# Kernel optimization log

Hardware: AMD Instinct MI355X
Metric: run time of the kernel (lower is better)

The kernel has to match this reference:

```python
import jax, jax.numpy as jnp
import numpy as np


def setup_inputs() -> dict:
    key = jax.random.key(0)
    ks = jax.random.split(key, 4)
    B, S, D, E = 8, 4096, 2048, 64
    scale = 1.0 / np.sqrt(D)
    return {
        "x": jax.random.normal(ks[0], (B, S, D), dtype=jnp.float32),
        "W_route": jax.random.normal(ks[1], (E, D), dtype=jnp.float32) * scale,
        "b_route": jnp.zeros((E,), dtype=jnp.float32),
        "W_noise": jax.random.normal(ks[2], (E, D), dtype=jnp.float32) * scale,
        "b_noise": jnp.zeros((E,), dtype=jnp.float32),
        "noise_eps": jax.random.normal(ks[3], (B, S, E), dtype=jnp.float32),
    }


TOP_K = 2


def reference(x, W_route, b_route, W_noise, b_noise, noise_eps):
    # Dual linear projections: [B,S,D] @ [D,E] -> [B,S,E]
    logits = jnp.einsum("bsd,ed->bse", x, W_route) + b_route
    noise_logits = jnp.einsum("bsd,ed->bse", x, W_noise) + b_noise
    noisy_logits = logits + noise_eps * jax.nn.softplus(noise_logits)

    B, S, E = noisy_logits.shape
    flat = noisy_logits.reshape(B * S, E)
    top_vals, top_idx = jax.lax.top_k(flat, TOP_K)  # [N,K]

    # Scatter top-k values into -inf background, then softmax over experts.
    neg_inf = jnp.full_like(flat, -jnp.inf)
    rows = jnp.arange(B * S)[:, None]
    sparse = neg_inf.at[rows, top_idx].set(top_vals)
    router_output = jax.nn.softmax(sparse, axis=-1).reshape(B, S, E)
    indices = top_idx.reshape(B, S, TOP_K)
    return router_output, indices
```

## Files before the change

kernel.cpp:

```cpp
#include <hip/hip_runtime.h>
#include <math.h>

typedef _Float16 f16;
typedef __attribute__((ext_vector_type(8))) _Float16 half8;
typedef __attribute__((ext_vector_type(4))) float f32x4;

#define NEXP 64
#define TM 64
#define L_STRIDE 132

__device__ __forceinline__ float softplus_f(float x) {
    return fmaxf(x, 0.0f) + log1pf(expf(-fabsf(x)));
}

__device__ __forceinline__ void lds_dma16(const void* g, void* l) {
    __builtin_amdgcn_global_load_lds(
        (const __attribute__((address_space(1))) unsigned int*)g,
        (__attribute__((address_space(3))) unsigned int*)l, 16, 0, 0);
}

__device__ __forceinline__ void cvt_split(const float4 a, const float4 b,
                                          half8& hv, half8& lv) {
    const float vv[8] = {a.x, a.y, a.z, a.w, b.x, b.y, b.z, b.w};
#pragma unroll
    for (int j = 0; j < 8; ++j) {
        const f16 h = (f16)vv[j];
        hv[j] = h;
        lv[j] = (f16)((vv[j] - (float)h) * 4096.0f);
    }
}

__global__ void wsplit_kernel(const float* __restrict__ Wr,
                              const float* __restrict__ Wn,
                              f16* __restrict__ ws, int D) {
    const int per_col = D >> 3;
    const int t = blockIdx.x * blockDim.x + threadIdx.x;
    const int col = t / per_col;
    const int k0  = (t - col * per_col) * 8;
    if (col >= 128) return;
    const float* src = (col < NEXP) ? &Wr[(size_t)col * D] : &Wn[(size_t)(col - NEXP) * D];
    const float4 v0 = *(const float4*)&src[k0];
    const float4 v1 = *(const float4*)&src[k0 + 4];
    half8 hi, lo;
    cvt_split(v0, v1, hi, lo);
    const int kc = k0 >> 5, q = (k0 >> 3) & 3;
    const size_t base = (size_t)kc * 8192 + (size_t)q * 1024 + (size_t)col * 8;
    *(half8*)&ws[base]        = hi;
    *(half8*)&ws[base + 4096] = lo;
}

__global__ __launch_bounds__(256, 3)
void router_mfma_kernel(const float* __restrict__ x,
                        const f16* __restrict__ wsW,
                        const float* __restrict__ br,
                        const float* __restrict__ bn,
                        const float* __restrict__ eps,
                        float* __restrict__ out,
                        int N, int D) {
    __shared__ union alignas(16) {
        struct { f16 B[2][8192]; f16 A[2][4096]; } st;
        float L[TM][L_STRIDE];
    } sm;
    __shared__ float biasLDS[128];
    __shared__ float p1s[TM], p2s[TM];
    __shared__ int   i1s[TM], i2s[TM];

    const int tid  = threadIdx.x;
    const int lane = tid & 63;
    const int w    = tid >> 6;
    const int rowbase = blockIdx.x * TM;
    const int wr = w & 1, wc = w >> 1;
    const int quad = lane >> 4;
    const int l16  = lane & 15;

    if (tid < 128) biasLDS[tid] = (tid < NEXP) ? br[tid] : bn[tid - NEXP];

    f32x4 accM[2][4], accC[2][4];
#pragma unroll
    for (int i = 0; i < 2; ++i)
#pragma unroll
        for (int j = 0; j < 4; ++j) {
            accM[i][j] = (f32x4){0.f, 0.f, 0.f, 0.f};
            accC[i][j] = (f32x4){0.f, 0.f, 0.f, 0.f};
        }

    const int sr = tid >> 2;
    const int sq = tid & 3;
    const float* xrow = &x[(size_t)(rowbase + sr) * D + sq * 8];
    const int nkc = D >> 5;

    float4 xva0, xva1, xvb0, xvb1;

    {
        const char* gsrc = (const char*)wsW + w * 4096 + lane * 16;
        char* ldst = (char*)&sm.st.B[0][0] + w * 4096;
#pragma unroll
        for (int i = 0; i < 4; ++i) lds_dma16(gsrc + i * 1024, ldst + i * 1024);
        __builtin_amdgcn_sched_barrier(0);
        const float4 c0a = *(const float4*)&xrow[0];
        const float4 c0b = *(const float4*)&xrow[4];
        __builtin_amdgcn_sched_barrier(0);
        xva0 = *(const float4*)&xrow[32];
        xva1 = *(const float4*)&xrow[36];
        xvb0 = *(const float4*)&xrow[64];
        xvb1 = *(const float4*)&xrow[68];
        __builtin_amdgcn_sched_barrier(0);
        half8 hv, lv;
        cvt_split(c0a, c0b, hv, lv);
        *(half8*)&sm.st.A[0][sq * 512 + sr * 8]        = hv;
        *(half8*)&sm.st.A[0][2048 + sq * 512 + sr * 8] = lv;
        asm volatile("s_waitcnt vmcnt(4) lgkmcnt(0)" : : : "memory");
        __builtin_amdgcn_s_barrier();
        __builtin_amdgcn_sched_barrier(0);
    }

#define KLOOP_BODY(KC, XV0, XV1)                                               \
    {                                                                          \
        const int cur = (KC) & 1, nxt = cur ^ 1;                               \
        if ((KC) + 1 < nkc) {                                                  \
            const char* gsrc = (const char*)wsW + (size_t)((KC) + 1) * 16384   \
                               + w * 4096 + lane * 16;                         \
            char* ldst = (char*)&sm.st.B[nxt][0] + w * 4096;                   \
            lds_dma16(gsrc,        ldst);                                      \
            lds_dma16(gsrc + 1024, ldst + 1024);                               \
            lds_dma16(gsrc + 2048, ldst + 2048);                               \
            lds_dma16(gsrc + 3072, ldst + 3072);                               \
        }                                                                      \
        __builtin_amdgcn_sched_barrier(0);                                     \
        if ((KC) + 1 < nkc) {                                                  \
            half8 hv, lv;                                                      \
            cvt_split(XV0, XV1, hv, lv);                                       \
            *(half8*)&sm.st.A[nxt][sq * 512 + sr * 8]        = hv;             \
            *(half8*)&sm.st.A[nxt][2048 + sq * 512 + sr * 8] = lv;             \
        }                                                                      \
        if ((KC) + 3 < nkc) {                                                  \
            XV0 = *(const float4*)&xrow[((KC) + 3) * 32];                      \
            XV1 = *(const float4*)&xrow[((KC) + 3) * 32 + 4];                  \
        }                                                                      \
        __builtin_amdgcn_sched_barrier(0);                                     \
        half8 ah[2], al[2], bh[4], bl[4];                                      \
        _Pragma("unroll")                                                      \
        for (int rt = 0; rt < 2; ++rt) {                                       \
            const int r = (wr * 32 + rt * 16 + l16) * 8;                       \
            ah[rt] = *(const half8*)&sm.st.A[cur][quad * 512 + r];             \
            al[rt] = *(const half8*)&sm.st.A[cur][2048 + quad * 512 + r];      \
        }                                                                      \
        _Pragma("unroll")                                                      \
        for (int ct = 0; ct < 4; ++ct) {                                       \
            const int c = (wc * 64 + ct * 16 + l16) * 8;                       \
            bh[ct] = *(const half8*)&sm.st.B[cur][quad * 1024 + c];            \
            bl[ct] = *(const half8*)&sm.st.B[cur][4096 + quad * 1024 + c];     \
        }                                                                      \
        _Pragma("unroll")                                                      \
        for (int rt = 0; rt < 2; ++rt)                                         \
            _Pragma("unroll")                                                  \
            for (int ct = 0; ct < 4; ++ct) {                                   \
                accM[rt][ct] = __builtin_amdgcn_mfma_f32_16x16x32_f16(         \
                    ah[rt], bh[ct], accM[rt][ct], 0, 0, 0);                    \
                accC[rt][ct] = __builtin_amdgcn_mfma_f32_16x16x32_f16(         \
                    al[rt], bh[ct], accC[rt][ct], 0, 0, 0);                    \
                accC[rt][ct] = __builtin_amdgcn_mfma_f32_16x16x32_f16(         \
                    ah[rt], bl[ct], accC[rt][ct], 0, 0, 0);                    \
            }                                                                  \
        if ((KC) + 3 < nkc)                                                    \
            asm volatile("s_waitcnt vmcnt(2) lgkmcnt(0)" : : : "memory");      \
        else                                                                   \
            asm volatile("s_waitcnt vmcnt(0) lgkmcnt(0)" : : : "memory");      \
        __builtin_amdgcn_s_barrier();                                          \
        __builtin_amdgcn_sched_barrier(0);                                     \
    }

    for (int kc = 0; kc < nkc; kc += 2) {
        KLOOP_BODY(kc,     xva0, xva1)
        KLOOP_BODY(kc + 1, xvb0, xvb1)
    }
#undef KLOOP_BODY

#pragma unroll
    for (int rt = 0; rt < 2; ++rt)
#pragma unroll
        for (int ct = 0; ct < 4; ++ct) {
            const int row = wr * 32 + rt * 16 + quad * 4;
            const int col = wc * 64 + ct * 16 + l16;
            const float bcol = biasLDS[col];
#pragma unroll
            for (int rg = 0; rg < 4; ++rg)
                sm.L[row + rg][col] = accM[rt][ct][rg] + accC[rt][ct][rg] * (1.0f / 4096.0f) + bcol;
        }
    __syncthreads();

#pragma unroll
    for (int t = 0; t < 4; ++t) {
        const int f   = tid * 4 + t * 1024;
        const int row = f >> 6;
        const int e0  = f & 63;
        const float4 ev = *(const float4*)&eps[(size_t)(rowbase + row) * NEXP + e0];
        const float evs[4] = {ev.x, ev.y, ev.z, ev.w};
#pragma unroll
        for (int j = 0; j < 4; ++j) {
            const float lg = sm.L[row][e0 + j];
            const float nz = sm.L[row][NEXP + e0 + j];
            sm.L[row][e0 + j] = fmaf(evs[j], softplus_f(nz), lg);
        }
    }
    __syncthreads();

    if (tid < TM) {
        const int r = tid;
        float v1t = -INFINITY, v2t = -INFINITY;
        int i1 = 0, i2 = 0;
#pragma unroll 8
        for (int e = 0; e < NEXP; ++e) {
            const float v = sm.L[r][e];
            if (v > v1t) { v2t = v1t; i2 = i1; v1t = v; i1 = e; }
            else if (v > v2t) { v2t = v; i2 = e; }
        }
        const float z = expf(v2t - v1t);
        const float s = 1.0f + z;
        p1s[r] = 1.0f / s;
        p2s[r] = z / s;
        i1s[r] = i1;
        i2s[r] = i2;
        float* oidx = out + (size_t)N * NEXP + (size_t)(rowbase + r) * 2;
        oidx[0] = (float)i1;
        oidx[1] = (float)i2;
    }
    __syncthreads();

    {
        const int r = tid >> 2;
        const int g = tid & 3;
        const float pa = p1s[r], pb = p2s[r];
        const int i1 = i1s[r], i2 = i2s[r];
        float* orow = out + (size_t)(rowbase + r) * NEXP;
#pragma unroll
        for (int t = 0; t < 4; ++t) {
            const int e0 = g * 16 + t * 4;
            float4 o;
            o.x = (e0 + 0 == i1) ? pa : ((e0 + 0 == i2) ? pb : 0.0f);
            o.y = (e0 + 1 == i1) ? pa : ((e0 + 1 == i2) ? pb : 0.0f);
            o.z = (e0 + 2 == i1) ? pa : ((e0 + 2 == i2) ? pb : 0.0f);
            o.w = (e0 + 3 == i1) ? pa : ((e0 + 3 == i2) ? pb : 0.0f);
            *(float4*)&orow[e0] = o;
        }
    }
}

#define BK 32
#define XS_STRIDE (TM + 4)
#define WS_STRIDE (128 + 4)

__global__ __launch_bounds__(256, 2)
void noisy_topk_router_kernel(const float* __restrict__ x,
                              const float* __restrict__ Wr,
                              const float* __restrict__ br,
                              const float* __restrict__ Wn,
                              const float* __restrict__ bn,
                              const float* __restrict__ eps,
                              float* __restrict__ out,
                              int N, int D) {
    __shared__ union alignas(16) {
        struct {
            float Xs[BK][XS_STRIDE];
            float Ws[BK][WS_STRIDE];
        } st;
        float L[TM][L_STRIDE];
    } sm;
    __shared__ float p1s[TM], p2s[TM];
    __shared__ int   i1s[TM], i2s[TM];

    const int tid = threadIdx.x;
    const int rowbase = blockIdx.x * TM;
    const int r0 = (tid >> 5) * 8;
    const int c0 = (tid & 31) * 4;

    float acc[8][4];
#pragma unroll
    for (int i = 0; i < 8; ++i)
#pragma unroll
        for (int j = 0; j < 4; ++j) acc[i][j] = 0.0f;

    const int q  = tid & 7;
    const int rr = tid >> 3;

    for (int k0 = 0; k0 < D; k0 += BK) {
#pragma unroll
        for (int i = 0; i < 2; ++i) {
            const int row = rr + 32 * i;
            const float4 xv = *(const float4*)&x[(size_t)(rowbase + row) * D + k0 + q * 4];
            sm.st.Xs[q * 4 + 0][row] = xv.x;
            sm.st.Xs[q * 4 + 1][row] = xv.y;
            sm.st.Xs[q * 4 + 2][row] = xv.z;
            sm.st.Xs[q * 4 + 3][row] = xv.w;
            const float4 wv = *(const float4*)&Wr[(size_t)row * D + k0 + q * 4];
            sm.st.Ws[q * 4 + 0][row] = wv.x;
            sm.st.Ws[q * 4 + 1][row] = wv.y;
            sm.st.Ws[q * 4 + 2][row] = wv.z;
            sm.st.Ws[q * 4 + 3][row] = wv.w;
            const float4 nv = *(const float4*)&Wn[(size_t)row * D + k0 + q * 4];
            sm.st.Ws[q * 4 + 0][NEXP + row] = nv.x;
            sm.st.Ws[q * 4 + 1][NEXP + row] = nv.y;
            sm.st.Ws[q * 4 + 2][NEXP + row] = nv.z;
            sm.st.Ws[q * 4 + 3][NEXP + row] = nv.w;
        }
        __syncthreads();
#pragma unroll 4
        for (int kk = 0; kk < BK; ++kk) {
            const float4 xa = *(const float4*)&sm.st.Xs[kk][r0];
            const float4 xb = *(const float4*)&sm.st.Xs[kk][r0 + 4];
            const float4 wv = *(const float4*)&sm.st.Ws[kk][c0];
            const float xs[8] = {xa.x, xa.y, xa.z, xa.w, xb.x, xb.y, xb.z, xb.w};
            const float ws[4] = {wv.x, wv.y, wv.z, wv.w};
#pragma unroll
            for (int i = 0; i < 8; ++i)
#pragma unroll
                for (int j = 0; j < 4; ++j)
                    acc[i][j] = fmaf(xs[i], ws[j], acc[i][j]);
        }
        __syncthreads();
    }
    {
        const float4 bv = (c0 < NEXP) ? *(const float4*)&br[c0]
                                      : *(const float4*)&bn[c0 - NEXP];
#pragma unroll
        for (int i = 0; i < 8; ++i) {
            float4 o;
            o.x = acc[i][0] + bv.x;
            o.y = acc[i][1] + bv.y;
            o.z = acc[i][2] + bv.z;
            o.w = acc[i][3] + bv.w;
            *(float4*)&sm.L[r0 + i][c0] = o;
        }
    }
    __syncthreads();
#pragma unroll
    for (int t = 0; t < 4; ++t) {
        const int f   = tid * 4 + t * 1024;
        const int row = f >> 6;
        const int e0  = f & 63;
        const float4 ev = *(const float4*)&eps[(size_t)(rowbase + row) * NEXP + e0];
        const float evs[4] = {ev.x, ev.y, ev.z, ev.w};
#pragma unroll
        for (int j = 0; j < 4; ++j) {
            const float lg = sm.L[row][e0 + j];
            const float nz = sm.L[row][NEXP + e0 + j];
            sm.L[row][e0 + j] = fmaf(evs[j], softplus_f(nz), lg);
        }
    }
    __syncthreads();
    if (tid < TM) {
        const int r = tid;
        float v1 = -INFINITY, v2 = -INFINITY;
        int i1 = 0, i2 = 0;
#pragma unroll 8
        for (int e = 0; e < NEXP; ++e) {
            const float v = sm.L[r][e];
            if (v > v1) { v2 = v1; i2 = i1; v1 = v; i1 = e; }
            else if (v > v2) { v2 = v; i2 = e; }
        }
        const float z = expf(v2 - v1);
        const float s = 1.0f + z;
        p1s[r] = 1.0f / s;
        p2s[r] = z / s;
        i1s[r] = i1;
        i2s[r] = i2;
        float* oidx = out + (size_t)N * NEXP + (size_t)(rowbase + r) * 2;
        oidx[0] = (float)i1;
        oidx[1] = (float)i2;
    }
    __syncthreads();
    {
        const int r = tid >> 2;
        const int g = tid & 3;
        const float pa = p1s[r], pb = p2s[r];
        const int i1 = i1s[r], i2 = i2s[r];
        float* orow = out + (size_t)(rowbase + r) * NEXP;
#pragma unroll
        for (int t = 0; t < 4; ++t) {
            const int e0 = g * 16 + t * 4;
            float4 o;
            o.x = (e0 + 0 == i1) ? pa : ((e0 + 0 == i2) ? pb : 0.0f);
            o.y = (e0 + 1 == i1) ? pa : ((e0 + 1 == i2) ? pb : 0.0f);
            o.z = (e0 + 2 == i1) ? pa : ((e0 + 2 == i2) ? pb : 0.0f);
            o.w = (e0 + 3 == i1) ? pa : ((e0 + 3 == i2) ? pb : 0.0f);
            *(float4*)&orow[e0] = o;
        }
    }
}

extern "C" void kernel_launch(void* const* d_in, const int* in_sizes, int n_in,
                              void* d_out, int out_size, void* d_ws, size_t ws_size,
                              hipStream_t stream) {
    const float* x   = (const float*)d_in[0];
    const float* Wr  = (const float*)d_in[1];
    const float* br  = (const float*)d_in[2];
    const float* Wn  = (const float*)d_in[3];
    const float* bn  = (const float*)d_in[4];
    const float* eps = (const float*)d_in[5];
    float* out = (float*)d_out;

    const int E = in_sizes[2];
    const int D = in_sizes[1] / E;
    const int N = in_sizes[0] / D;

    const size_t ws_needed = (size_t)128 * D * 2 * sizeof(f16);
    const bool fast = (E == 64) && (D == 2048) && (N % TM == 0) && (ws_size >= ws_needed);

    if (fast) {
        const int pre_threads = 128 * (D / 8);
        wsplit_kernel<<<(pre_threads + 255) / 256, 256, 0, stream>>>(Wr, Wn, (f16*)d_ws, D);
        router_mfma_kernel<<<N / TM, 256, 0, stream>>>(x, (const f16*)d_ws, br, bn, eps, out, N, D);
    } else {
        noisy_topk_router_kernel<<<N / TM, 256, 0, stream>>>(x, Wr, br, Wn, bn, eps, out, N, D);
    }
}
```

Measured before the change: 429.9 us.

## Load MFMA operands directly from global into registers, dropping LDS staging and barriers

The k-loop no longer stages x and the split-f16 weights through double-buffered LDS with DMA loads and per-step barriers. Each wave now loads its own A rows (as fp32, converted to hi/lo f16 in registers) and B fragments straight from global memory, using register double-buffering across even and odd k-chunks. The goal is to remove block-wide synchronisation and LDS traffic from the inner loop. The cost is that each x row and each weight fragment is fetched by two waves, which doubles L2 traffic and raises register pressure; launch bounds drop from 3 to 2 blocks per SM to make room.

```diff
diff --git a/kernel.cpp b/kernel.cpp
--- a/kernel.cpp
+++ b/kernel.cpp
@@ -11,12 +11,6 @@
 
 __device__ __forceinline__ float softplus_f(float x) {
     return fmaxf(x, 0.0f) + log1pf(expf(-fabsf(x)));
-}
-
-__device__ __forceinline__ void lds_dma16(const void* g, void* l) {
-    __builtin_amdgcn_global_load_lds(
-        (const __attribute__((address_space(1))) unsigned int*)g,
-        (__attribute__((address_space(3))) unsigned int*)l, 16, 0, 0);
 }
 
 __device__ __forceinline__ void cvt_split(const float4 a, const float4 b,
@@ -49,7 +43,7 @@
     *(half8*)&ws[base + 4096] = lo;
 }
 
-__global__ __launch_bounds__(256, 3)
+__global__ __launch_bounds__(256, 2)
 void router_mfma_kernel(const float* __restrict__ x,
                         const f16* __restrict__ wsW,
                         const float* __restrict__ br,
@@ -57,10 +51,7 @@
                         const float* __restrict__ eps,
                         float* __restrict__ out,
                         int N, int D) {
-    __shared__ union alignas(16) {
-        struct { f16 B[2][8192]; f16 A[2][4096]; } st;
-        float L[TM][L_STRIDE];
-    } sm;
+    __shared__ float L[TM][L_STRIDE];
     __shared__ float biasLDS[128];
     __shared__ float p1s[TM], p2s[TM];
     __shared__ int   i1s[TM], i2s[TM];
@@ -84,73 +75,36 @@
             accC[i][j] = (f32x4){0.f, 0.f, 0.f, 0.f};
         }
 
-    const int sr = tid >> 2;
-    const int sq = tid & 3;
-    const float* xrow = &x[(size_t)(rowbase + sr) * D + sq * 8];
+    const float* xA0 = x + (size_t)(rowbase + wr * 32 + l16) * D + quad * 8;
+    const float* xA1 = xA0 + (size_t)16 * D;
+    const f16* bsrc = wsW + quad * 1024 + (size_t)(wc * 64 + l16) * 8;
+
     const int nkc = D >> 5;
 
-    float4 xva0, xva1, xvb0, xvb1;
-
-    {
-        const char* gsrc = (const char*)wsW + w * 4096 + lane * 16;
-        char* ldst = (char*)&sm.st.B[0][0] + w * 4096;
-#pragma unroll
-        for (int i = 0; i < 4; ++i) lds_dma16(gsrc + i * 1024, ldst + i * 1024);
-        __builtin_amdgcn_sched_barrier(0);
-        const float4 c0a = *(const float4*)&xrow[0];
-        const float4 c0b = *(const float4*)&xrow[4];
-        __builtin_amdgcn_sched_barrier(0);
-        xva0 = *(const float4*)&xrow[32];
-        xva1 = *(const float4*)&xrow[36];
-        xvb0 = *(const float4*)&xrow[64];
-        xvb1 = *(const float4*)&xrow[68];
-        __builtin_amdgcn_sched_barrier(0);
-        half8 hv, lv;
-        cvt_split(c0a, c0b, hv, lv);
-        *(half8*)&sm.st.A[0][sq * 512 + sr * 8]        = hv;
-        *(half8*)&sm.st.A[0][2048 + sq * 512 + sr * 8] = lv;
-        asm volatile("s_waitcnt vmcnt(4) lgkmcnt(0)" : : : "memory");
-        __builtin_amdgcn_s_barrier();
-        __builtin_amdgcn_sched_barrier(0);
-    }
-
-#define KLOOP_BODY(KC, XV0, XV1)                                               \
+    float4 aE00 = *(const float4*)&xA0[0];
+    float4 aE01 = *(const float4*)&xA0[4];
+    float4 aE10 = *(const float4*)&xA1[0];
+    float4 aE11 = *(const float4*)&xA1[4];
+    float4 aO00 = *(const float4*)&xA0[32];
+    float4 aO01 = *(const float4*)&xA0[36];
+    float4 aO10 = *(const float4*)&xA1[32];
+    float4 aO11 = *(const float4*)&xA1[36];
+    half8 bhE0 = *(const half8*)&bsrc[0];
+    half8 bhE1 = *(const half8*)&bsrc[128];
+    half8 bhE2 = *(const half8*)&bsrc[256];
+    half8 bhE3 = *(const half8*)&bsrc[384];
+    half8 blE0 = *(const half8*)&bsrc[4096];
+    half8 blE1 = *(const half8*)&bsrc[4224];
+    half8 blE2 = *(const half8*)&bsrc[4352];
+    half8 blE3 = *(const half8*)&bsrc[4480];
+    half8 bhO0, bhO1, bhO2, bhO3, blO0, blO1, blO2, blO3;
+
+#define MFMA_BLOCK(AH0, AL0, AH1, AL1, BH0, BH1, BH2, BH3, BL0, BL1, BL2, BL3) \
     {                                                                          \
-        const int cur = (KC) & 1, nxt = cur ^ 1;                               \
-        if ((KC) + 1 < nkc) {                                                  \
-            const char* gsrc = (const char*)wsW + (size_t)((KC) + 1) * 16384   \
-                               + w * 4096 + lane * 16;                         \
-            char* ldst = (char*)&sm.st.B[nxt][0] + w * 4096;                   \
-            lds_dma16(gsrc,        ldst);                                      \
-            lds_dma16(gsrc + 1024, ldst + 1024);                               \
-            lds_dma16(gsrc + 2048, ldst + 2048);                               \
-            lds_dma16(gsrc + 3072, ldst + 3072);                               \
-        }                                                                      \
-        __builtin_amdgcn_sched_barrier(0);                                     \
-        if ((KC) + 1 < nkc) {                                                  \
-            half8 hv, lv;                                                      \
-            cvt_split(XV0, XV1, hv, lv);                                       \
-            *(half8*)&sm.st.A[nxt][sq * 512 + sr * 8]        = hv;             \
-            *(half8*)&sm.st.A[nxt][2048 + sq * 512 + sr * 8] = lv;             \
-        }                                                                      \
-        if ((KC) + 3 < nkc) {                                                  \
-            XV0 = *(const float4*)&xrow[((KC) + 3) * 32];                      \
-            XV1 = *(const float4*)&xrow[((KC) + 3) * 32 + 4];                  \
-        }                                                                      \
-        __builtin_amdgcn_sched_barrier(0);                                     \
         half8 ah[2], al[2], bh[4], bl[4];                                      \
-        _Pragma("unroll")                                                      \
-        for (int rt = 0; rt < 2; ++rt) {                                       \
-            const int r = (wr * 32 + rt * 16 + l16) * 8;                       \
-            ah[rt] = *(const half8*)&sm.st.A[cur][quad * 512 + r];             \
-            al[rt] = *(const half8*)&sm.st.A[cur][2048 + quad * 512 + r];      \
-        }                                                                      \
-        _Pragma("unroll")                                                      \
-        for (int ct = 0; ct < 4; ++ct) {                                       \
-            const int c = (wc * 64 + ct * 16 + l16) * 8;                       \
-            bh[ct] = *(const half8*)&sm.st.B[cur][quad * 1024 + c];            \
-            bl[ct] = *(const half8*)&sm.st.B[cur][4096 + quad * 1024 + c];     \
-        }                                                                      \
+        ah[0] = AH0; al[0] = AL0; ah[1] = AH1; al[1] = AL1;                    \
+        bh[0] = BH0; bh[1] = BH1; bh[2] = BH2; bh[3] = BH3;                    \
+        bl[0] = BL0; bl[1] = BL1; bl[2] = BL2; bl[3] = BL3;                    \
         _Pragma("unroll")                                                      \
         for (int rt = 0; rt < 2; ++rt)                                         \
             _Pragma("unroll")                                                  \
@@ -162,19 +116,59 @@
                 accC[rt][ct] = __builtin_amdgcn_mfma_f32_16x16x32_f16(         \
                     ah[rt], bl[ct], accC[rt][ct], 0, 0, 0);                    \
             }                                                                  \
-        if ((KC) + 3 < nkc)                                                    \
-            asm volatile("s_waitcnt vmcnt(2) lgkmcnt(0)" : : : "memory");      \
-        else                                                                   \
-            asm volatile("s_waitcnt vmcnt(0) lgkmcnt(0)" : : : "memory");      \
-        __builtin_amdgcn_s_barrier();                                          \
-        __builtin_amdgcn_sched_barrier(0);                                     \
     }
 
     for (int kc = 0; kc < nkc; kc += 2) {
-        KLOOP_BODY(kc,     xva0, xva1)
-        KLOOP_BODY(kc + 1, xvb0, xvb1)
-    }
-#undef KLOOP_BODY
+        {
+            const int ia = (kc + 2 < nkc) ? (kc + 2) : (nkc - 1);
+            const int ib = (kc + 1 < nkc) ? (kc + 1) : (nkc - 1);
+            const f16* bp = bsrc + (size_t)ib * 8192;
+            bhO0 = *(const half8*)&bp[0];
+            bhO1 = *(const half8*)&bp[128];
+            bhO2 = *(const half8*)&bp[256];
+            bhO3 = *(const half8*)&bp[384];
+            blO0 = *(const half8*)&bp[4096];
+            blO1 = *(const half8*)&bp[4224];
+            blO2 = *(const half8*)&bp[4352];
+            blO3 = *(const half8*)&bp[4480];
+            const float* p0 = xA0 + ia * 32;
+            const float* p1 = xA1 + ia * 32;
+            half8 ah0, al0, ah1, al1;
+            cvt_split(aE00, aE01, ah0, al0);
+            cvt_split(aE10, aE11, ah1, al1);
+            aE00 = *(const float4*)&p0[0];
+            aE01 = *(const float4*)&p0[4];
+            aE10 = *(const float4*)&p1[0];
+            aE11 = *(const float4*)&p1[4];
+            MFMA_BLOCK(ah0, al0, ah1, al1, bhE0, bhE1, bhE2, bhE3,
+                       blE0, blE1, blE2, blE3)
+        }
+        {
+            const int ia = (kc + 3 < nkc) ? (kc + 3) : (nkc - 1);
+            const int ib = (kc + 2 < nkc) ? (kc + 2) : (nkc - 1);
+            const f16* bp = bsrc + (size_t)ib * 8192;
+            bhE0 = *(const half8*)&bp[0];
+            bhE1 = *(const half8*)&bp[128];
+            bhE2 = *(const half8*)&bp[256];
+            bhE3 = *(const half8*)&bp[384];
+            blE0 = *(const half8*)&bp[4096];
+            blE1 = *(const half8*)&bp[4224];
+            blE2 = *(const half8*)&bp[4352];
+            blE3 = *(const half8*)&bp[4480];
+            const float* p0 = xA0 + ia * 32;
+            const float* p1 = xA1 + ia * 32;
+            half8 ah0, al0, ah1, al1;
+            cvt_split(aO00, aO01, ah0, al0);
+            cvt_split(aO10, aO11, ah1, al1);
+            aO00 = *(const float4*)&p0[0];
+            aO01 = *(const float4*)&p0[4];
+            aO10 = *(const float4*)&p1[0];
+            aO11 = *(const float4*)&p1[4];
+            MFMA_BLOCK(ah0, al0, ah1, al1, bhO0, bhO1, bhO2, bhO3,
+                       blO0, blO1, blO2, blO3)
+        }
+    }
+#undef MFMA_BLOCK
 
 #pragma unroll
     for (int rt = 0; rt < 2; ++rt)
@@ -185,7 +179,7 @@
             const float bcol = biasLDS[col];
 #pragma unroll
             for (int rg = 0; rg < 4; ++rg)
-                sm.L[row + rg][col] = accM[rt][ct][rg] + accC[rt][ct][rg] * (1.0f / 4096.0f) + bcol;
+                L[row + rg][col] = accM[rt][ct][rg] + accC[rt][ct][rg] * (1.0f / 4096.0f) + bcol;
         }
     __syncthreads();
 
@@ -198,9 +192,9 @@
         const float evs[4] = {ev.x, ev.y, ev.z, ev.w};
 #pragma unroll
         for (int j = 0; j < 4; ++j) {
-            const float lg = sm.L[row][e0 + j];
-            const float nz = sm.L[row][NEXP + e0 + j];
-            sm.L[row][e0 + j] = fmaf(evs[j], softplus_f(nz), lg);
+            const float lg = L[row][e0 + j];
+            const float nz = L[row][NEXP + e0 + j];
+            L[row][e0 + j] = fmaf(evs[j], softplus_f(nz), lg);
         }
     }
     __syncthreads();
@@ -211,7 +205,7 @@
         int i1 = 0, i2 = 0;
 #pragma unroll 8
         for (int e = 0; e < NEXP; ++e) {
-            const float v = sm.L[r][e];
+            const float v = L[r][e];
             if (v > v1t) { v2t = v1t; i2 = i1; v1t = v; i1 = e; }
             else if (v > v2t) { v2t = v; i2 = e; }
         }
```

After: 529.1 us. +23.1%, slower.

## Halve row tile, load x fragments directly to registers, drop A staging in LDS

Applied to the files above, without the earlier changes.

Shrinks the row tile per block from 64 to 32, so each wave handles a single 16-row MFMA tile. Each lane now loads its x fragment straight from global memory into registers and converts it to fp16 hi/lo there, removing the A staging buffer and its LDS writes and reads. The smaller LDS footprint lets launch bounds rise to 4 blocks per CU and doubles the grid. In exchange, the W tile in LDS is reused across fewer rows per block, so there is more LDS DMA traffic per output row, and the x loads are less coalesced.

```diff
diff --git a/kernel.cpp b/kernel.cpp
--- a/kernel.cpp
+++ b/kernel.cpp
@@ -6,6 +6,7 @@
 typedef __attribute__((ext_vector_type(4))) float f32x4;
 
 #define NEXP 64
+#define TMR 32
 #define TM 64
 #define L_STRIDE 132
 
@@ -49,7 +50,7 @@
     *(half8*)&ws[base + 4096] = lo;
 }
 
-__global__ __launch_bounds__(256, 3)
+__global__ __launch_bounds__(256, 4)
 void router_mfma_kernel(const float* __restrict__ x,
                         const f16* __restrict__ wsW,
                         const float* __restrict__ br,
@@ -58,111 +59,87 @@
                         float* __restrict__ out,
                         int N, int D) {
     __shared__ union alignas(16) {
-        struct { f16 B[2][8192]; f16 A[2][4096]; } st;
-        float L[TM][L_STRIDE];
+        f16 B[2][8192];
+        struct {
+            float L[TMR][L_STRIDE];
+            float p1[TMR], p2[TMR];
+            int   i1[TMR], i2[TMR];
+        } ep;
     } sm;
-    __shared__ float biasLDS[128];
-    __shared__ float p1s[TM], p2s[TM];
-    __shared__ int   i1s[TM], i2s[TM];
 
     const int tid  = threadIdx.x;
     const int lane = tid & 63;
     const int w    = tid >> 6;
-    const int rowbase = blockIdx.x * TM;
+    const int rowbase = blockIdx.x * TMR;
     const int wr = w & 1, wc = w >> 1;
     const int quad = lane >> 4;
     const int l16  = lane & 15;
 
-    if (tid < 128) biasLDS[tid] = (tid < NEXP) ? br[tid] : bn[tid - NEXP];
-
-    f32x4 accM[2][4], accC[2][4];
-#pragma unroll
-    for (int i = 0; i < 2; ++i)
-#pragma unroll
-        for (int j = 0; j < 4; ++j) {
-            accM[i][j] = (f32x4){0.f, 0.f, 0.f, 0.f};
-            accC[i][j] = (f32x4){0.f, 0.f, 0.f, 0.f};
-        }
-
-    const int sr = tid >> 2;
-    const int sq = tid & 3;
-    const float* xrow = &x[(size_t)(rowbase + sr) * D + sq * 8];
+    f32x4 accM[4], accC[4];
+#pragma unroll
+    for (int j = 0; j < 4; ++j) {
+        accM[j] = (f32x4){0.f, 0.f, 0.f, 0.f};
+        accC[j] = (f32x4){0.f, 0.f, 0.f, 0.f};
+    }
+
+    const float* xA = x + (size_t)(rowbase + wr * 16 + l16) * D + quad * 8;
     const int nkc = D >> 5;
 
-    float4 xva0, xva1, xvb0, xvb1;
+    float4 aE0, aE1, aO0, aO1;
 
     {
         const char* gsrc = (const char*)wsW + w * 4096 + lane * 16;
-        char* ldst = (char*)&sm.st.B[0][0] + w * 4096;
+        char* ldst = (char*)&sm.B[0][0] + w * 4096;
 #pragma unroll
         for (int i = 0; i < 4; ++i) lds_dma16(gsrc + i * 1024, ldst + i * 1024);
         __builtin_amdgcn_sched_barrier(0);
-        const float4 c0a = *(const float4*)&xrow[0];
-        const float4 c0b = *(const float4*)&xrow[4];
+        aE0 = *(const float4*)&xA[0];
+        aE1 = *(const float4*)&xA[4];
+        aO0 = *(const float4*)&xA[32];
+        aO1 = *(const float4*)&xA[36];
         __builtin_amdgcn_sched_barrier(0);
-        xva0 = *(const float4*)&xrow[32];
-        xva1 = *(const float4*)&xrow[36];
-        xvb0 = *(const float4*)&xrow[64];
-        xvb1 = *(const float4*)&xrow[68];
-        __builtin_amdgcn_sched_barrier(0);
-        half8 hv, lv;
-        cvt_split(c0a, c0b, hv, lv);
-        *(half8*)&sm.st.A[0][sq * 512 + sr * 8]        = hv;
-        *(half8*)&sm.st.A[0][2048 + sq * 512 + sr * 8] = lv;
-        asm volatile("s_waitcnt vmcnt(4) lgkmcnt(0)" : : : "memory");
+        asm volatile("s_waitcnt vmcnt(4)" : : : "memory");
         __builtin_amdgcn_s_barrier();
         __builtin_amdgcn_sched_barrier(0);
     }
 
-#define KLOOP_BODY(KC, XV0, XV1)                                               \
+#define KLOOP_BODY(KC, A0, A1)                                                 \
     {                                                                          \
         const int cur = (KC) & 1, nxt = cur ^ 1;                               \
         if ((KC) + 1 < nkc) {                                                  \
             const char* gsrc = (const char*)wsW + (size_t)((KC) + 1) * 16384   \
                                + w * 4096 + lane * 16;                         \
-            char* ldst = (char*)&sm.st.B[nxt][0] + w * 4096;                   \
+            char* ldst = (char*)&sm.B[nxt][0] + w * 4096;                      \
             lds_dma16(gsrc,        ldst);                                      \
             lds_dma16(gsrc + 1024, ldst + 1024);                               \
             lds_dma16(gsrc + 2048, ldst + 2048);                               \
             lds_dma16(gsrc + 3072, ldst + 3072);                               \
         }                                                                      \
         __builtin_amdgcn_sched_barrier(0);                                     \
-        if ((KC) + 1 < nkc) {                                                  \
-            half8 hv, lv;                                                      \
-            cvt_split(XV0, XV1, hv, lv);                                       \
-            *(half8*)&sm.st.A[nxt][sq * 512 + sr * 8]        = hv;             \
-            *(half8*)&sm.st.A[nxt][2048 + sq * 512 + sr * 8] = lv;             \
-        }                                                                      \
-        if ((KC) + 3 < nkc) {                                                  \
-            XV0 = *(const float4*)&xrow[((KC) + 3) * 32];                      \
-            XV1 = *(const float4*)&xrow[((KC) + 3) * 32 + 4];                  \
+        half8 ah, al;                                                          \
+        cvt_split(A0, A1, ah, al);                                             \
+        if ((KC) + 2 < nkc) {                                                  \
+            A0 = *(const float4*)&xA[((KC) + 2) * 32];                         \
+            A1 = *(const float4*)&xA[((KC) + 2) * 32 + 4];                     \
         }                                                                      \
         __builtin_amdgcn_sched_barrier(0);                                     \
-        half8 ah[2], al[2], bh[4], bl[4];                                      \
+        half8 bh[4], bl[4];                                                    \
         _Pragma("unroll")                                                      \
-        for (int rt = 0; rt < 2; ++rt) {                                       \
-            const int r = (wr * 32 + rt * 16 + l16) * 8;                       \
-            ah[rt] = *(const half8*)&sm.st.A[cur][quad * 512 + r];             \
-            al[rt] = *(const half8*)&sm.st.A[cur][2048 + quad * 512 + r];      \
+        for (int ct = 0; ct < 4; ++ct) {                                       \
+            const int c = (wc * 64 + ct * 16 + l16) * 8;                       \
+            bh[ct] = *(const half8*)&sm.B[cur][quad * 1024 + c];               \
+            bl[ct] = *(const half8*)&sm.B[cur][4096 + quad * 1024 + c];        \
         }                                                                      \
         _Pragma("unroll")                                                      \
         for (int ct = 0; ct < 4; ++ct) {                                       \
-            const int c = (wc * 64 + ct * 16 + l16) * 8;                       \
-            bh[ct] = *(const half8*)&sm.st.B[cur][quad * 1024 + c];            \
-            bl[ct] = *(const half8*)&sm.st.B[cur][4096 + quad * 1024 + c];     \
+            accM[ct] = __builtin_amdgcn_mfma_f32_16x16x32_f16(                 \
+                ah, bh[ct], accM[ct], 0, 0, 0);                                \
+            accC[ct] = __builtin_amdgcn_mfma_f32_16x16x32_f16(                 \
+                al, bh[ct], accC[ct], 0, 0, 0);                                \
+            accC[ct] = __builtin_amdgcn_mfma_f32_16x16x32_f16(                 \
+                ah, bl[ct], accC[ct], 0, 0, 0);                                \
         }                                                                      \
-        _Pragma("unroll")                                                      \
-        for (int rt = 0; rt < 2; ++rt)                                         \
-            _Pragma("unroll")                                                  \
-            for (int ct = 0; ct < 4; ++ct) {                                   \
-                accM[rt][ct] = __builtin_amdgcn_mfma_f32_16x16x32_f16(         \
-                    ah[rt], bh[ct], accM[rt][ct], 0, 0, 0);                    \
-                accC[rt][ct] = __builtin_amdgcn_mfma_f32_16x16x32_f16(         \
-                    al[rt], bh[ct], accC[rt][ct], 0, 0, 0);                    \
-                accC[rt][ct] = __builtin_amdgcn_mfma_f32_16x16x32_f16(         \
-                    ah[rt], bl[ct], accC[rt][ct], 0, 0, 0);                    \
-            }                                                                  \
-        if ((KC) + 3 < nkc)                                                    \
+        if ((KC) + 2 < nkc)                                                    \
             asm volatile("s_waitcnt vmcnt(2) lgkmcnt(0)" : : : "memory");      \
         else                                                                   \
             asm volatile("s_waitcnt vmcnt(0) lgkmcnt(0)" : : : "memory");      \
@@ -171,26 +148,28 @@
     }
 
     for (int kc = 0; kc < nkc; kc += 2) {
-        KLOOP_BODY(kc,     xva0, xva1)
-        KLOOP_BODY(kc + 1, xvb0, xvb1)
+        KLOOP_BODY(kc,     aE0, aE1)
+        KLOOP_BODY(kc + 1, aO0, aO1)
     }
 #undef KLOOP_BODY
 
-#pragma unroll
-    for (int rt = 0; rt < 2; ++rt)
+    {
+        const float* bias = wc ? bn : br;
+        const int row = wr * 16 + quad * 4;
 #pragma unroll
         for (int ct = 0; ct < 4; ++ct) {
-            const int row = wr * 32 + rt * 16 + quad * 4;
             const int col = wc * 64 + ct * 16 + l16;
-            const float bcol = biasLDS[col];
+            const float bcol = bias[ct * 16 + l16];
 #pragma unroll
             for (int rg = 0; rg < 4; ++rg)
-                sm.L[row + rg][col] = accM[rt][ct][rg] + accC[rt][ct][rg] * (1.0f / 4096.0f) + bcol;
-        }
-    __syncthreads();
-
-#pragma unroll
-    for (int t = 0; t < 4; ++t) {
+                sm.ep.L[row + rg][col] =
+                    accM[ct][rg] + accC[ct][rg] * (1.0f / 4096.0f) + bcol;
+        }
+    }
+    __syncthreads();
+
+#pragma unroll
+    for (int t = 0; t < 2; ++t) {
         const int f   = tid * 4 + t * 1024;
         const int row = f >> 6;
         const int e0  = f & 63;
@@ -198,29 +177,29 @@
         const float evs[4] = {ev.x, ev.y, ev.z, ev.w};
 #pragma unroll
         for (int j = 0; j < 4; ++j) {
-            const float lg = sm.L[row][e0 + j];
-            const float nz = sm.L[row][NEXP + e0 + j];
-            sm.L[row][e0 + j] = fmaf(evs[j], softplus_f(nz), lg);
-        }
-    }
-    __syncthreads();
-
-    if (tid < TM) {
+            const float lg = sm.ep.L[row][e0 + j];
+            const float nz = sm.ep.L[row][NEXP + e0 + j];
+            sm.ep.L[row][e0 + j] = fmaf(evs[j], softplus_f(nz), lg);
+        }
+    }
+    __syncthreads();
+
+    if (tid < TMR) {
         const int r = tid;
         float v1t = -INFINITY, v2t = -INFINITY;
         int i1 = 0, i2 = 0;
 #pragma unroll 8
         for (int e = 0; e < NEXP; ++e) {
-            const float v = sm.L[r][e];
+            const float v = sm.ep.L[r][e];
             if (v > v1t) { v2t = v1t; i2 = i1; v1t = v; i1 = e; }
             else if (v > v2t) { v2t = v; i2 = e; }
         }
         const float z = expf(v2t - v1t);
         const float s = 1.0f + z;
-        p1s[r] = 1.0f / s;
-        p2s[r] = z / s;
-        i1s[r] = i1;
-        i2s[r] = i2;
+        sm.ep.p1[r] = 1.0f / s;
+        sm.ep.p2[r] = z / s;
+        sm.ep.i1[r] = i1;
+        sm.ep.i2[r] = i2;
         float* oidx = out + (size_t)N * NEXP + (size_t)(rowbase + r) * 2;
         oidx[0] = (float)i1;
         oidx[1] = (float)i2;
@@ -228,14 +207,14 @@
     __syncthreads();
 
     {
-        const int r = tid >> 2;
-        const int g = tid & 3;
-        const float pa = p1s[r], pb = p2s[r];
-        const int i1 = i1s[r], i2 = i2s[r];
+        const int r = tid >> 3;
+        const int g = tid & 7;
+        const float pa = sm.ep.p1[r], pb = sm.ep.p2[r];
+        const int i1 = sm.ep.i1[r], i2 = sm.ep.i2[r];
         float* orow = out + (size_t)(rowbase + r) * NEXP;
 #pragma unroll
-        for (int t = 0; t < 4; ++t) {
-            const int e0 = g * 16 + t * 4;
+        for (int t = 0; t < 2; ++t) {
+            const int e0 = g * 8 + t * 4;
             float4 o;
             o.x = (e0 + 0 == i1) ? pa : ((e0 + 0 == i2) ? pb : 0.0f);
             o.y = (e0 + 1 == i1) ? pa : ((e0 + 1 == i2) ? pb : 0.0f);
@@ -404,12 +383,12 @@
     const int N = in_sizes[0] / D;
 
     const size_t ws_needed = (size_t)128 * D * 2 * sizeof(f16);
-    const bool fast = (E == 64) && (D == 2048) && (N % TM == 0) && (ws_size >= ws_needed);
+    const bool fast = (E == 64) && (D == 2048) && (N % TMR == 0) && (ws_size >= ws_needed);
 
     if (fast) {
         const int pre_threads = 128 * (D / 8);
         wsplit_kernel<<<(pre_threads + 255) / 256, 256, 0, stream>>>(Wr, Wn, (f16*)d_ws, D);
-        router_mfma_kernel<<<N / TM, 256, 0, stream>>>(x, (const f16*)d_ws, br, bn, eps, out, N, D);
+        router_mfma_kernel<<<N / TMR, 256, 0, stream>>>(x, (const f16*)d_ws, br, bn, eps, out, N, D);
     } else {
         noisy_topk_router_kernel<<<N / TM, 256, 0, stream>>>(x, Wr, br, Wn, bn, eps, out, N, D);
     }
```

After: 433.5 us. No clear change (+0.8%).

## Triple-buffer weight tiles to prefetch two K-chunks ahead

Applied to the files above, without the earlier changes.

Weight tiles now go through three LDS buffers with a rotating buffer index, so the DMA for chunk k+2 is issued while chunk k is computed, and the wait counts are retuned to match. The prologue issues two weight chunks up front. The bias LDS staging is dropped in favour of direct global reads, and the epilogue scratch arrays move into the LDS union. Larger LDS use lowers the occupancy hint from 3 to 2 blocks per CU, trading occupancy for deeper latency hiding.

```diff
diff --git a/kernel.cpp b/kernel.cpp
--- a/kernel.cpp
+++ b/kernel.cpp
@@ -49,7 +49,7 @@
     *(half8*)&ws[base + 4096] = lo;
 }
 
-__global__ __launch_bounds__(256, 3)
+__global__ __launch_bounds__(256, 2)
 void router_mfma_kernel(const float* __restrict__ x,
                         const f16* __restrict__ wsW,
                         const float* __restrict__ br,
@@ -58,12 +58,13 @@
                         float* __restrict__ out,
                         int N, int D) {
     __shared__ union alignas(16) {
-        struct { f16 B[2][8192]; f16 A[2][4096]; } st;
-        float L[TM][L_STRIDE];
+        struct { f16 B[3][8192]; f16 A[3][4096]; } st;
+        struct {
+            float L[TM][L_STRIDE];
+            float p1[TM], p2[TM];
+            int   i1[TM], i2[TM];
+        } ep;
     } sm;
-    __shared__ float biasLDS[128];
-    __shared__ float p1s[TM], p2s[TM];
-    __shared__ int   i1s[TM], i2s[TM];
 
     const int tid  = threadIdx.x;
     const int lane = tid & 63;
@@ -73,8 +74,6 @@
     const int quad = lane >> 4;
     const int l16  = lane & 15;
 
-    if (tid < 128) biasLDS[tid] = (tid < NEXP) ? br[tid] : bn[tid - NEXP];
-
     f32x4 accM[2][4], accC[2][4];
 #pragma unroll
     for (int i = 0; i < 2; ++i)
@@ -89,24 +88,27 @@
     const float* xrow = &x[(size_t)(rowbase + sr) * D + sq * 8];
     const int nkc = D >> 5;
 
-    float4 xva0, xva1, xvb0, xvb1;
+    float4 xe0, xe1, xo0, xo1;
 
     {
-        const char* gsrc = (const char*)wsW + w * 4096 + lane * 16;
-        char* ldst = (char*)&sm.st.B[0][0] + w * 4096;
-#pragma unroll
-        for (int i = 0; i < 4; ++i) lds_dma16(gsrc + i * 1024, ldst + i * 1024);
+        const float4 t0 = *(const float4*)&xrow[0];
+        const float4 t1 = *(const float4*)&xrow[4];
+        xe0 = *(const float4*)&xrow[32];
+        xe1 = *(const float4*)&xrow[36];
+        xo0 = *(const float4*)&xrow[64];
+        xo1 = *(const float4*)&xrow[68];
         __builtin_amdgcn_sched_barrier(0);
-        const float4 c0a = *(const float4*)&xrow[0];
-        const float4 c0b = *(const float4*)&xrow[4];
-        __builtin_amdgcn_sched_barrier(0);
-        xva0 = *(const float4*)&xrow[32];
-        xva1 = *(const float4*)&xrow[36];
-        xvb0 = *(const float4*)&xrow[64];
-        xvb1 = *(const float4*)&xrow[68];
+        const char* g0 = (const char*)wsW + w * 4096 + lane * 16;
+        char* d0 = (char*)&sm.st.B[0][0] + w * 4096;
+#pragma unroll
+        for (int i = 0; i < 4; ++i) lds_dma16(g0 + i * 1024, d0 + i * 1024);
+        const char* g1 = (const char*)wsW + 16384 + w * 4096 + lane * 16;
+        char* d1 = (char*)&sm.st.B[1][0] + w * 4096;
+#pragma unroll
+        for (int i = 0; i < 4; ++i) lds_dma16(g1 + i * 1024, d1 + i * 1024);
         __builtin_amdgcn_sched_barrier(0);
         half8 hv, lv;
-        cvt_split(c0a, c0b, hv, lv);
+        cvt_split(t0, t1, hv, lv);
         *(half8*)&sm.st.A[0][sq * 512 + sr * 8]        = hv;
         *(half8*)&sm.st.A[0][2048 + sq * 512 + sr * 8] = lv;
         asm volatile("s_waitcnt vmcnt(4) lgkmcnt(0)" : : : "memory");
@@ -114,42 +116,47 @@
         __builtin_amdgcn_sched_barrier(0);
     }
 
-#define KLOOP_BODY(KC, XV0, XV1)                                               \
+    int bC = 0, bA = 1, bS = 2;
+
+#define KBODY(KC, X0, X1)                                                      \
     {                                                                          \
-        const int cur = (KC) & 1, nxt = cur ^ 1;                               \
+                              \
         if ((KC) + 1 < nkc) {                                                  \
-            const char* gsrc = (const char*)wsW + (size_t)((KC) + 1) * 16384   \
+            half8 hv, lv;                                                      \
+            cvt_split(X0, X1, hv, lv);                                         \
+            *(half8*)&sm.st.A[bA][sq * 512 + sr * 8]        = hv;              \
+            *(half8*)&sm.st.A[bA][2048 + sq * 512 + sr * 8] = lv;              \
+        }                                                                      \
+        __builtin_amdgcn_sched_barrier(0);                                     \
+                \
+        if ((KC) + 2 < nkc) {                                                  \
+            const char* gsrc = (const char*)wsW + (size_t)((KC) + 2) * 16384   \
                                + w * 4096 + lane * 16;                         \
-            char* ldst = (char*)&sm.st.B[nxt][0] + w * 4096;                   \
+            char* ldst = (char*)&sm.st.B[bS][0] + w * 4096;                    \
             lds_dma16(gsrc,        ldst);                                      \
             lds_dma16(gsrc + 1024, ldst + 1024);                               \
             lds_dma16(gsrc + 2048, ldst + 2048);                               \
             lds_dma16(gsrc + 3072, ldst + 3072);                               \
         }                                                                      \
         __builtin_amdgcn_sched_barrier(0);                                     \
-        if ((KC) + 1 < nkc) {                                                  \
-            half8 hv, lv;                                                      \
-            cvt_split(XV0, XV1, hv, lv);                                       \
-            *(half8*)&sm.st.A[nxt][sq * 512 + sr * 8]        = hv;             \
-            *(half8*)&sm.st.A[nxt][2048 + sq * 512 + sr * 8] = lv;             \
-        }                                                                      \
+                       \
         if ((KC) + 3 < nkc) {                                                  \
-            XV0 = *(const float4*)&xrow[((KC) + 3) * 32];                      \
-            XV1 = *(const float4*)&xrow[((KC) + 3) * 32 + 4];                  \
+            X0 = *(const float4*)&xrow[((KC) + 3) * 32];                       \
+            X1 = *(const float4*)&xrow[((KC) + 3) * 32 + 4];                   \
         }                                                                      \
         __builtin_amdgcn_sched_barrier(0);                                     \
         half8 ah[2], al[2], bh[4], bl[4];                                      \
         _Pragma("unroll")                                                      \
         for (int rt = 0; rt < 2; ++rt) {                                       \
             const int r = (wr * 32 + rt * 16 + l16) * 8;                       \
-            ah[rt] = *(const half8*)&sm.st.A[cur][quad * 512 + r];             \
-            al[rt] = *(const half8*)&sm.st.A[cur][2048 + quad * 512 + r];      \
+            ah[rt] = *(const half8*)&sm.st.A[bC][quad * 512 + r];              \
+            al[rt] = *(const half8*)&sm.st.A[bC][2048 + quad * 512 + r];       \
         }                                                                      \
         _Pragma("unroll")                                                      \
         for (int ct = 0; ct < 4; ++ct) {                                       \
             const int c = (wc * 64 + ct * 16 + l16) * 8;                       \
-            bh[ct] = *(const half8*)&sm.st.B[cur][quad * 1024 + c];            \
-            bl[ct] = *(const half8*)&sm.st.B[cur][4096 + quad * 1024 + c];     \
+            bh[ct] = *(const half8*)&sm.st.B[bC][quad * 1024 + c];             \
+            bl[ct] = *(const half8*)&sm.st.B[bC][4096 + quad * 1024 + c];      \
         }                                                                      \
         _Pragma("unroll")                                                      \
         for (int rt = 0; rt < 2; ++rt)                                         \
@@ -162,31 +169,39 @@
                 accC[rt][ct] = __builtin_amdgcn_mfma_f32_16x16x32_f16(         \
                     ah[rt], bl[ct], accC[rt][ct], 0, 0, 0);                    \
             }                                                                  \
-        if ((KC) + 3 < nkc)                                                    \
-            asm volatile("s_waitcnt vmcnt(2) lgkmcnt(0)" : : : "memory");      \
+           \
+        if ((KC) == 0)                                                         \
+            asm volatile("s_waitcnt vmcnt(6) lgkmcnt(0)" : : : "memory");      \
+        else if ((KC) + 4 < nkc)                                               \
+            asm volatile("s_waitcnt vmcnt(8) lgkmcnt(0)" : : : "memory");      \
         else                                                                   \
             asm volatile("s_waitcnt vmcnt(0) lgkmcnt(0)" : : : "memory");      \
         __builtin_amdgcn_s_barrier();                                          \
         __builtin_amdgcn_sched_barrier(0);                                     \
+        { const int t_ = bC; bC = bA; bA = bS; bS = t_; }                      \
     }
 
     for (int kc = 0; kc < nkc; kc += 2) {
-        KLOOP_BODY(kc,     xva0, xva1)
-        KLOOP_BODY(kc + 1, xvb0, xvb1)
-    }
-#undef KLOOP_BODY
-
-#pragma unroll
-    for (int rt = 0; rt < 2; ++rt)
-#pragma unroll
-        for (int ct = 0; ct < 4; ++ct) {
-            const int row = wr * 32 + rt * 16 + quad * 4;
-            const int col = wc * 64 + ct * 16 + l16;
-            const float bcol = biasLDS[col];
-#pragma unroll
-            for (int rg = 0; rg < 4; ++rg)
-                sm.L[row + rg][col] = accM[rt][ct][rg] + accC[rt][ct][rg] * (1.0f / 4096.0f) + bcol;
-        }
+        KBODY(kc,     xe0, xe1)
+        KBODY(kc + 1, xo0, xo1)
+    }
+#undef KBODY
+
+    {
+        const float* bias = wc ? bn : br;
+#pragma unroll
+        for (int rt = 0; rt < 2; ++rt)
+#pragma unroll
+            for (int ct = 0; ct < 4; ++ct) {
+                const int row = wr * 32 + rt * 16 + quad * 4;
+                const int col = wc * 64 + ct * 16 + l16;
+                const float bcol = bias[ct * 16 + l16];
+#pragma unroll
+                for (int rg = 0; rg < 4; ++rg)
+                    sm.ep.L[row + rg][col] =
+                        accM[rt][ct][rg] + accC[rt][ct][rg] * (1.0f / 4096.0f) + bcol;
+            }
+    }
     __syncthreads();
 
 #pragma unroll
@@ -198,9 +213,9 @@
         const float evs[4] = {ev.x, ev.y, ev.z, ev.w};
 #pragma unroll
         for (int j = 0; j < 4; ++j) {
-            const float lg = sm.L[row][e0 + j];
-            const float nz = sm.L[row][NEXP + e0 + j];
-            sm.L[row][e0 + j] = fmaf(evs[j], softplus_f(nz), lg);
+            const float lg = sm.ep.L[row][e0 + j];
+            const float nz = sm.ep.L[row][NEXP + e0 + j];
+            sm.ep.L[row][e0 + j] = fmaf(evs[j], softplus_f(nz), lg);
         }
     }
     __syncthreads();
@@ -211,16 +226,16 @@
         int i1 = 0, i2 = 0;
 #pragma unroll 8
         for (int e = 0; e < NEXP; ++e) {
-            const float v = sm.L[r][e];
+            const float v = sm.ep.L[r][e];
             if (v > v1t) { v2t = v1t; i2 = i1; v1t = v; i1 = e; }
             else if (v > v2t) { v2t = v; i2 = e; }
         }
         const float z = expf(v2t - v1t);
         const float s = 1.0f + z;
-        p1s[r] = 1.0f / s;
-        p2s[r] = z / s;
-        i1s[r] = i1;
-        i2s[r] = i2;
+        sm.ep.p1[r] = 1.0f / s;
+        sm.ep.p2[r] = z / s;
+        sm.ep.i1[r] = i1;
+        sm.ep.i2[r] = i2;
         float* oidx = out + (size_t)N * NEXP + (size_t)(rowbase + r) * 2;
         oidx[0] = (float)i1;
         oidx[1] = (float)i2;
@@ -230,8 +245,8 @@
     {
         const int r = tid >> 2;
         const int g = tid & 3;
-        const float pa = p1s[r], pb = p2s[r];
-        const int i1 = i1s[r], i2 = i2s[r];
+        const float pa = sm.ep.p1[r], pb = sm.ep.p2[r];
+        const int i1 = sm.ep.i1[r], i2 = sm.ep.i2[r];
         float* orow = out + (size_t)(rowbase + r) * NEXP;
 #pragma unroll
         for (int t = 0; t < 4; ++t) {
```

Measured after the change: 408.4 us. 5.0% less time.
